# Performance work log

Measured on AMD Instinct MI355X. Metric: run time of the kernel, lower is better.

## Reference

```python
import jax, jax.numpy as jnp
import numpy as np

B, S, D, M = 4, 4096, 2048, 512

def _xavier(k, shape):
    return jax.random.normal(k, shape, jnp.float32) * np.float32(np.sqrt(2.0 / (shape[0] + shape[1])))

def setup_inputs() -> dict:
    key = jax.random.key(0)
    ks = jax.random.split(key, 6)
    return dict(
        x=jax.random.normal(ks[0], (B, S, D), jnp.float32),
        memory_state=jnp.zeros((B, M), jnp.float32),
        Wk=_xavier(ks[1], (M, D)), bk=jnp.zeros((M,), jnp.float32),
        Wv=_xavier(ks[2], (M, D)), bv=jnp.zeros((M,), jnp.float32),
        Wg=_xavier(ks[3], (D, D + M)), bg=jnp.zeros((D,), jnp.float32),
        time_decay=jax.random.normal(ks[4], (M,), jnp.float32) * 0.01,
        time_first=jax.random.normal(ks[5], (M,), jnp.float32) * 0.01,
    )

def reference(x, memory_state, Wk, bk, Wv, bv, Wg, bg, time_decay, time_first):
    # decay in (0.1, 1.0) per channel
    td = jax.nn.sigmoid(time_decay) * 0.9 + 0.1          # (M,)
    tf = jax.nn.sigmoid(time_first)                      # (M,)
    # k is computed but never used in the source forward; kept for FLOP parity
    k = jnp.einsum('bsd,md->bsm', x, Wk) + bk
    v = jnp.einsum('bsd,md->bsm', x, Wv) + bv            # (B,S,M)
    # sum_{j<=i} td^(i-j) * v_j  ==  linear recurrence s_i = td*s_{i-1} + v_i
    def step(s, v_t):
        s = td * s + v_t
        return s, s
    _, wv = jax.lax.scan(step, jnp.zeros((x.shape[0], td.shape[0]), x.dtype),
                         jnp.swapaxes(v, 0, 1))          # (S,B,M)
    wv = jnp.swapaxes(wv, 0, 1) + memory_state[:, None, :] * tf  # (B,S,M)
    next_memory_state = wv[:, -1]                        # taken before dropout (eval: identity)
    combined = jnp.concatenate([x, wv], axis=-1)         # (B,S,D+M)
    out = x + jnp.einsum('bse,de->bsd', combined, Wg) + bg
    return out, next_memory_state
```

## Files before the change

kernel.cpp:

```cpp
#include <hip/hip_runtime.h>
#include <hip/hip_bf16.h>
#include <stdint.h>

#define B_ 4
#define S_ 4096
#define D_ 2048
#define M_ 512
#define E_ (D_ + M_)
#define BS_ (B_ * S_)
#define CH_ 32
#define CL_ 128

typedef __attribute__((ext_vector_type(8))) short short8;
typedef __attribute__((ext_vector_type(4))) short short4e;
typedef __attribute__((ext_vector_type(4))) float float4e;

__device__ __forceinline__ unsigned short f2bf(float f) {
    unsigned int u = __float_as_uint(f);
    u = (u + 0x7fffu + ((u >> 16) & 1u)) >> 16;
    return (unsigned short)u;
}

__device__ __forceinline__ float sigmoidf(float x) {
    return 1.0f / (1.0f + expf(-x));
}

__device__ __forceinline__ void load_lds16(const unsigned short* g, unsigned short* l) {
    __builtin_amdgcn_global_load_lds(
        (const __attribute__((address_space(1))) unsigned int*)g,
        (__attribute__((address_space(3))) unsigned int*)l,
        16, 0, 0);
}

__global__ void conv_x_kernel(const float* __restrict__ x, unsigned short* __restrict__ comb) {
    int i = blockIdx.x * blockDim.x + threadIdx.x;
    const int n4 = BS_ * D_ / 4;
    const int stride = gridDim.x * blockDim.x;
    for (; i < n4; i += stride) {
        int flat = i << 2;
        int row = flat >> 11;
        int col = flat & (D_ - 1);
        float4 xv = ((const float4*)x)[i];
        short4e o = { (short)f2bf(xv.x), (short)f2bf(xv.y),
                      (short)f2bf(xv.z), (short)f2bf(xv.w) };
        *(short4e*)(comb + (size_t)row * E_ + col) = o;
    }
}

__global__ void conv_gen(const float* __restrict__ in, unsigned short* __restrict__ out, int n4) {
    int i = blockIdx.x * blockDim.x + threadIdx.x;
    const int stride = gridDim.x * blockDim.x;
    for (; i < n4; i += stride) {
        float4 xv = ((const float4*)in)[i];
        short4e o = { (short)f2bf(xv.x), (short)f2bf(xv.y),
                      (short)f2bf(xv.z), (short)f2bf(xv.w) };
        ((short4e*)out)[i] = o;
    }
}

template<bool ADDX>
__global__ __launch_bounds__(256) void gemm_bt(
    const unsigned short* __restrict__ A, int lda,
    const unsigned short* __restrict__ Bm, int ldb,
    float* __restrict__ C, int ldc,
    const float* __restrict__ bias,
    const float* __restrict__ xres,
    int K)
{
    __shared__ unsigned short As[128 * 64];
    __shared__ unsigned short Bs[128 * 64];

    const int tid  = threadIdx.x;
    const int lane = tid & 63;
    const int wave = __builtin_amdgcn_readfirstlane(tid >> 6);
    const int bm0  = blockIdx.x * 128;
    const int bn0  = blockIdx.y * 128;
    const int wm   = wave & 1;
    const int wn   = wave >> 1;
    const int lm   = lane & 15;
    const int quad = lane >> 4;

    const unsigned short* ag[4];
    const unsigned short* bgp[4];
    unsigned short* al[4];
    unsigned short* bl[4];
#pragma unroll
    for (int i = 0; i < 4; ++i) {
        int g = i * 256 + tid;
        int r = g >> 3, c = g & 7;
        int cg = c ^ (r & 7);
        ag[i]  = A  + (size_t)(bm0 + r) * lda + cg * 8;
        bgp[i] = Bm + (size_t)(bn0 + r) * ldb + cg * 8;
        int lg = i * 256 + wave * 64;
        al[i] = As + lg * 8;
        bl[i] = Bs + lg * 8;
    }

    float4e acc[4][4];
    const float4e zero = {0.f, 0.f, 0.f, 0.f};
#pragma unroll
    for (int i = 0; i < 4; ++i)
#pragma unroll
        for (int j = 0; j < 4; ++j) acc[i][j] = zero;

    for (int k0 = 0; k0 < K; k0 += 64) {
#pragma unroll
        for (int i = 0; i < 4; ++i) {
            load_lds16(ag[i]  + k0, al[i]);
            load_lds16(bgp[i] + k0, bl[i]);
        }
        __syncthreads();
#pragma unroll
        for (int kk = 0; kk < 2; ++kk) {
            short8 af[4], bf[4];
#pragma unroll
            for (int i = 0; i < 4; ++i) {
                int ra = wm * 64 + i * 16 + lm;
                af[i] = *(const short8*)(As + ra * 64 + (((kk * 4 + quad) ^ (ra & 7)) * 8));
                int rb = wn * 64 + i * 16 + lm;
                bf[i] = *(const short8*)(Bs + rb * 64 + (((kk * 4 + quad) ^ (rb & 7)) * 8));
            }
#pragma unroll
            for (int i = 0; i < 4; ++i)
#pragma unroll
                for (int j = 0; j < 4; ++j)
                    acc[i][j] = __builtin_amdgcn_mfma_f32_16x16x32_bf16(af[i], bf[j], acc[i][j], 0, 0, 0);
        }
        __syncthreads();
    }

#pragma unroll
    for (int i = 0; i < 4; ++i) {
#pragma unroll
        for (int j = 0; j < 4; ++j) {
            int row = bm0 + wm * 64 + i * 16 + quad * 4;
            int col = bn0 + wn * 64 + j * 16 + lm;
            float bb = bias[col];
#pragma unroll
            for (int r = 0; r < 4; ++r) {
                size_t idx = (size_t)(row + r) * ldc + col;
                float val = acc[i][j][r] + bb;
                if (ADDX) val += xres[idx];
                C[idx] = val;
            }
        }
    }
}

__global__ void scan_p1(const float* __restrict__ v, const float* __restrict__ tdp,
                        float* __restrict__ Ebuf) {
    int tid = blockIdx.x * blockDim.x + threadIdx.x;
    int m = tid & (M_ - 1);
    int c = (tid >> 9) & (CH_ - 1);
    int b = tid >> 14;
    float td = 0.9f * sigmoidf(tdp[m]) + 0.1f;
    const float* vp = v + (size_t)(b * S_ + c * CL_) * M_ + m;
    float s = 0.f;
#pragma unroll 4
    for (int t = 0; t < CL_; ++t) s = td * s + vp[(size_t)t * M_];
    Ebuf[(b * CH_ + c) * M_ + m] = s;
}

__global__ void scan_p2(const float* __restrict__ tdp, const float* __restrict__ Ebuf,
                        float* __restrict__ Sbuf) {
    int tid = blockIdx.x * blockDim.x + threadIdx.x;
    int m = tid & (M_ - 1);
    int b = tid >> 9;
    float td = 0.9f * sigmoidf(tdp[m]) + 0.1f;
    float a = td;
#pragma unroll
    for (int i = 0; i < 7; ++i) a *= a;
    float s = 0.f;
    for (int c = 0; c < CH_; ++c) {
        Sbuf[(b * CH_ + c) * M_ + m] = s;
        s = a * s + Ebuf[(b * CH_ + c) * M_ + m];
    }
}

__global__ void scan_p3(const float* __restrict__ v, const float* __restrict__ tdp,
                        const float* __restrict__ tfp, const float* __restrict__ ms,
                        const float* __restrict__ Sbuf, unsigned short* __restrict__ comb,
                        float* __restrict__ out_state) {
    int tid = blockIdx.x * blockDim.x + threadIdx.x;
    int m = tid & (M_ - 1);
    int c = (tid >> 9) & (CH_ - 1);
    int b = tid >> 14;
    float td  = 0.9f * sigmoidf(tdp[m]) + 0.1f;
    float add = ms[b * M_ + m] * sigmoidf(tfp[m]);
    float s   = Sbuf[(b * CH_ + c) * M_ + m];
    const float* vp = v + (size_t)(b * S_ + c * CL_) * M_ + m;
    unsigned short* cp = comb + (size_t)(b * S_ + c * CL_) * E_ + D_ + m;
    float w = 0.f;
#pragma unroll 4
    for (int t = 0; t < CL_; ++t) {
        s = td * s + vp[(size_t)t * M_];
        w = s + add;
        cp[(size_t)t * E_] = f2bf(w);
    }
    if (c == CH_ - 1) out_state[b * M_ + m] = w;
}

extern "C" void kernel_launch(void* const* d_in, const int* in_sizes, int n_in,
                              void* d_out, int out_size, void* d_ws, size_t ws_size,
                              hipStream_t stream) {
    const float* x    = (const float*)d_in[0];
    const float* ms   = (const float*)d_in[1];
    const float* Wv   = (const float*)d_in[4];
    const float* bv   = (const float*)d_in[5];
    const float* Wg   = (const float*)d_in[6];
    const float* bg   = (const float*)d_in[7];
    const float* tdec = (const float*)d_in[8];
    const float* tfir = (const float*)d_in[9];

    float* out       = (float*)d_out;
    float* out_state = out + (size_t)BS_ * D_;

    char* ws = (char*)d_ws;
    size_t off = 0;
    unsigned short* comb = (unsigned short*)(ws + off); off += (size_t)BS_ * E_ * 2;
    float*          vbuf = (float*)(ws + off);          off += (size_t)BS_ * M_ * 4;
    unsigned short* Wvb  = (unsigned short*)(ws + off); off += (size_t)M_ * D_ * 2;
    unsigned short* Wgb  = (unsigned short*)(ws + off); off += (size_t)D_ * E_ * 2;
    float*          Ebuf = (float*)(ws + off);          off += (size_t)B_ * CH_ * M_ * 4;
    float*          Sbuf = (float*)(ws + off);          off += (size_t)B_ * CH_ * M_ * 4;

    conv_x_kernel<<<4096, 256, 0, stream>>>(x, comb);
    conv_gen<<<512, 256, 0, stream>>>(Wv, Wvb, M_ * D_ / 4);
    conv_gen<<<2048, 256, 0, stream>>>(Wg, Wgb, D_ * E_ / 4);

    gemm_bt<false><<<dim3(BS_ / 128, M_ / 128), 256, 0, stream>>>(
        comb, E_, Wvb, D_, vbuf, M_, bv, nullptr, D_);

    scan_p1<<<(B_ * CH_ * M_) / 256, 256, 0, stream>>>(vbuf, tdec, Ebuf);
    scan_p2<<<(B_ * M_) / 256, 256, 0, stream>>>(tdec, Ebuf, Sbuf);
    scan_p3<<<(B_ * CH_ * M_) / 256, 256, 0, stream>>>(vbuf, tdec, tfir, ms, Sbuf, comb, out_state);

    gemm_bt<true><<<dim3(BS_ / 128, D_ / 128), 256, 0, stream>>>(
        comb, E_, Wgb, E_, out, D_, bg, x, E_);
}
```

Before: 581.5 us.

## Store v in bf16, merge weight casts, fold scan pass 2, read residual from bf16

Several changes ship together. The v projection now writes bf16 instead of fp32 and uses 128x64 tiles, which halves the traffic the scan kernels read. The two weight-cast kernels become one launch, and the scan's middle pass is removed by having each chunk recompute its carry-in prefix. The output GEMM reads the x residual from the bf16 copy in comb instead of fp32 x, and its grid is reordered so N varies fastest. These cut memory traffic and launches, but rounding v and the residual x to bf16 lowers accuracy; the residual loss in particular may break tolerance.

```diff
diff --git a/kernel.cpp b/kernel.cpp
--- a/kernel.cpp
+++ b/kernel.cpp
@@ -20,7 +20,9 @@
     u = (u + 0x7fffu + ((u >> 16) & 1u)) >> 16;
     return (unsigned short)u;
 }
-
+__device__ __forceinline__ float bf2f(unsigned short h) {
+    return __uint_as_float(((unsigned int)h) << 16);
+}
 __device__ __forceinline__ float sigmoidf(float x) {
     return 1.0f / (1.0f + expf(-x));
 }
@@ -47,155 +49,165 @@
     }
 }
 
-__global__ void conv_gen(const float* __restrict__ in, unsigned short* __restrict__ out, int n4) {
+__global__ void conv_w_kernel(const float* __restrict__ Wv, unsigned short* __restrict__ Wvb,
+                              const float* __restrict__ Wg, unsigned short* __restrict__ Wgb) {
+    const int nv4 = M_ * D_ / 4;
+    const int ng4 = D_ * E_ / 4;
     int i = blockIdx.x * blockDim.x + threadIdx.x;
     const int stride = gridDim.x * blockDim.x;
-    for (; i < n4; i += stride) {
-        float4 xv = ((const float4*)in)[i];
+    for (; i < nv4 + ng4; i += stride) {
+        const float* in;
+        unsigned short* out;
+        int j;
+        if (i < nv4) { in = Wv; out = Wvb; j = i; }
+        else         { in = Wg; out = Wgb; j = i - nv4; }
+        float4 xv = ((const float4*)in)[j];
         short4e o = { (short)f2bf(xv.x), (short)f2bf(xv.y),
                       (short)f2bf(xv.z), (short)f2bf(xv.w) };
-        ((short4e*)out)[i] = o;
-    }
-}
-
-template<bool ADDX>
+        ((short4e*)out)[j] = o;
+    }
+}
+
+template<int BM, int BN, bool ADDX, bool OUT_BF16>
 __global__ __launch_bounds__(256) void gemm_bt(
     const unsigned short* __restrict__ A, int lda,
     const unsigned short* __restrict__ Bm, int ldb,
-    float* __restrict__ C, int ldc,
+    void* __restrict__ Cv, int ldc,
     const float* __restrict__ bias,
-    const float* __restrict__ xres,
+    const unsigned short* __restrict__ resid, int resid_ld,
     int K)
 {
-    __shared__ unsigned short As[128 * 64];
-    __shared__ unsigned short Bs[128 * 64];
+    constexpr int MI = BM / 32;
+    constexpr int NJ = BN / 32;
+    constexpr int NGA = BM / 32;
+    constexpr int NGB = BN / 32;
+
+    __shared__ unsigned short As[BM * 64];
+    __shared__ unsigned short Bs[BN * 64];
 
     const int tid  = threadIdx.x;
     const int lane = tid & 63;
     const int wave = __builtin_amdgcn_readfirstlane(tid >> 6);
-    const int bm0  = blockIdx.x * 128;
-    const int bn0  = blockIdx.y * 128;
+    const int bn0  = blockIdx.x * BN;
+    const int bm0  = blockIdx.y * BM;
     const int wm   = wave & 1;
     const int wn   = wave >> 1;
     const int lm   = lane & 15;
     const int quad = lane >> 4;
 
-    const unsigned short* ag[4];
-    const unsigned short* bgp[4];
-    unsigned short* al[4];
-    unsigned short* bl[4];
-#pragma unroll
-    for (int i = 0; i < 4; ++i) {
+    const unsigned short* ag[NGA];
+    unsigned short* al[NGA];
+#pragma unroll
+    for (int i = 0; i < NGA; ++i) {
         int g = i * 256 + tid;
         int r = g >> 3, c = g & 7;
         int cg = c ^ (r & 7);
-        ag[i]  = A  + (size_t)(bm0 + r) * lda + cg * 8;
+        ag[i] = A + (size_t)(bm0 + r) * lda + cg * 8;
+        al[i] = As + (i * 256 + wave * 64) * 8;
+    }
+    const unsigned short* bgp[NGB];
+    unsigned short* bl[NGB];
+#pragma unroll
+    for (int i = 0; i < NGB; ++i) {
+        int g = i * 256 + tid;
+        int r = g >> 3, c = g & 7;
+        int cg = c ^ (r & 7);
         bgp[i] = Bm + (size_t)(bn0 + r) * ldb + cg * 8;
-        int lg = i * 256 + wave * 64;
-        al[i] = As + lg * 8;
-        bl[i] = Bs + lg * 8;
-    }
-
-    float4e acc[4][4];
+        bl[i] = Bs + (i * 256 + wave * 64) * 8;
+    }
+
+    float4e acc[MI][NJ];
     const float4e zero = {0.f, 0.f, 0.f, 0.f};
 #pragma unroll
-    for (int i = 0; i < 4; ++i)
-#pragma unroll
-        for (int j = 0; j < 4; ++j) acc[i][j] = zero;
+    for (int i = 0; i < MI; ++i)
+#pragma unroll
+        for (int j = 0; j < NJ; ++j) acc[i][j] = zero;
 
     for (int k0 = 0; k0 < K; k0 += 64) {
 #pragma unroll
-        for (int i = 0; i < 4; ++i) {
-            load_lds16(ag[i]  + k0, al[i]);
-            load_lds16(bgp[i] + k0, bl[i]);
-        }
+        for (int i = 0; i < NGA; ++i) load_lds16(ag[i] + k0, al[i]);
+#pragma unroll
+        for (int i = 0; i < NGB; ++i) load_lds16(bgp[i] + k0, bl[i]);
         __syncthreads();
 #pragma unroll
         for (int kk = 0; kk < 2; ++kk) {
-            short8 af[4], bf[4];
-#pragma unroll
-            for (int i = 0; i < 4; ++i) {
-                int ra = wm * 64 + i * 16 + lm;
+            short8 af[MI], bf[NJ];
+#pragma unroll
+            for (int i = 0; i < MI; ++i) {
+                int ra = wm * (BM / 2) + i * 16 + lm;
                 af[i] = *(const short8*)(As + ra * 64 + (((kk * 4 + quad) ^ (ra & 7)) * 8));
-                int rb = wn * 64 + i * 16 + lm;
-                bf[i] = *(const short8*)(Bs + rb * 64 + (((kk * 4 + quad) ^ (rb & 7)) * 8));
             }
 #pragma unroll
-            for (int i = 0; i < 4; ++i)
-#pragma unroll
-                for (int j = 0; j < 4; ++j)
+            for (int j = 0; j < NJ; ++j) {
+                int rb = wn * (BN / 2) + j * 16 + lm;
+                bf[j] = *(const short8*)(Bs + rb * 64 + (((kk * 4 + quad) ^ (rb & 7)) * 8));
+            }
+#pragma unroll
+            for (int i = 0; i < MI; ++i)
+#pragma unroll
+                for (int j = 0; j < NJ; ++j)
                     acc[i][j] = __builtin_amdgcn_mfma_f32_16x16x32_bf16(af[i], bf[j], acc[i][j], 0, 0, 0);
         }
         __syncthreads();
     }
 
 #pragma unroll
-    for (int i = 0; i < 4; ++i) {
-#pragma unroll
-        for (int j = 0; j < 4; ++j) {
-            int row = bm0 + wm * 64 + i * 16 + quad * 4;
-            int col = bn0 + wn * 64 + j * 16 + lm;
+    for (int i = 0; i < MI; ++i) {
+#pragma unroll
+        for (int j = 0; j < NJ; ++j) {
+            int row = bm0 + wm * (BM / 2) + i * 16 + quad * 4;
+            int col = bn0 + wn * (BN / 2) + j * 16 + lm;
             float bb = bias[col];
 #pragma unroll
             for (int r = 0; r < 4; ++r) {
                 size_t idx = (size_t)(row + r) * ldc + col;
                 float val = acc[i][j][r] + bb;
-                if (ADDX) val += xres[idx];
-                C[idx] = val;
+                if (ADDX) val += bf2f(resid[(size_t)(row + r) * resid_ld + col]);
+                if (OUT_BF16) ((unsigned short*)Cv)[idx] = f2bf(val);
+                else          ((float*)Cv)[idx] = val;
             }
         }
     }
 }
 
-__global__ void scan_p1(const float* __restrict__ v, const float* __restrict__ tdp,
+__global__ void scan_p1(const unsigned short* __restrict__ v, const float* __restrict__ tdp,
                         float* __restrict__ Ebuf) {
     int tid = blockIdx.x * blockDim.x + threadIdx.x;
     int m = tid & (M_ - 1);
     int c = (tid >> 9) & (CH_ - 1);
     int b = tid >> 14;
     float td = 0.9f * sigmoidf(tdp[m]) + 0.1f;
-    const float* vp = v + (size_t)(b * S_ + c * CL_) * M_ + m;
+    const unsigned short* vp = v + (size_t)(b * S_ + c * CL_) * M_ + m;
     float s = 0.f;
 #pragma unroll 4
-    for (int t = 0; t < CL_; ++t) s = td * s + vp[(size_t)t * M_];
+    for (int t = 0; t < CL_; ++t) s = td * s + bf2f(vp[(size_t)t * M_]);
     Ebuf[(b * CH_ + c) * M_ + m] = s;
 }
 
-__global__ void scan_p2(const float* __restrict__ tdp, const float* __restrict__ Ebuf,
-                        float* __restrict__ Sbuf) {
-    int tid = blockIdx.x * blockDim.x + threadIdx.x;
-    int m = tid & (M_ - 1);
-    int b = tid >> 9;
-    float td = 0.9f * sigmoidf(tdp[m]) + 0.1f;
-    float a = td;
-#pragma unroll
-    for (int i = 0; i < 7; ++i) a *= a;
-    float s = 0.f;
-    for (int c = 0; c < CH_; ++c) {
-        Sbuf[(b * CH_ + c) * M_ + m] = s;
-        s = a * s + Ebuf[(b * CH_ + c) * M_ + m];
-    }
-}
-
-__global__ void scan_p3(const float* __restrict__ v, const float* __restrict__ tdp,
+__global__ void scan_p3(const unsigned short* __restrict__ v, const float* __restrict__ tdp,
                         const float* __restrict__ tfp, const float* __restrict__ ms,
-                        const float* __restrict__ Sbuf, unsigned short* __restrict__ comb,
+                        const float* __restrict__ Ebuf, unsigned short* __restrict__ comb,
                         float* __restrict__ out_state) {
     int tid = blockIdx.x * blockDim.x + threadIdx.x;
     int m = tid & (M_ - 1);
     int c = (tid >> 9) & (CH_ - 1);
     int b = tid >> 14;
     float td  = 0.9f * sigmoidf(tdp[m]) + 0.1f;
+    float a = td;
+#pragma unroll
+    for (int i = 0; i < 7; ++i) a *= a;
+    float s = 0.f;
+    for (int cp = 0; cp < c; ++cp)
+        s = a * s + Ebuf[(b * CH_ + cp) * M_ + m];
     float add = ms[b * M_ + m] * sigmoidf(tfp[m]);
-    float s   = Sbuf[(b * CH_ + c) * M_ + m];
-    const float* vp = v + (size_t)(b * S_ + c * CL_) * M_ + m;
-    unsigned short* cp = comb + (size_t)(b * S_ + c * CL_) * E_ + D_ + m;
+    const unsigned short* vp = v + (size_t)(b * S_ + c * CL_) * M_ + m;
+    unsigned short* cp_ = comb + (size_t)(b * S_ + c * CL_) * E_ + D_ + m;
     float w = 0.f;
 #pragma unroll 4
     for (int t = 0; t < CL_; ++t) {
-        s = td * s + vp[(size_t)t * M_];
+        s = td * s + bf2f(vp[(size_t)t * M_]);
         w = s + add;
-        cp[(size_t)t * E_] = f2bf(w);
+        cp_[(size_t)t * E_] = f2bf(w);
     }
     if (c == CH_ - 1) out_state[b * M_ + m] = w;
 }
@@ -218,23 +230,20 @@
     char* ws = (char*)d_ws;
     size_t off = 0;
     unsigned short* comb = (unsigned short*)(ws + off); off += (size_t)BS_ * E_ * 2;
-    float*          vbuf = (float*)(ws + off);          off += (size_t)BS_ * M_ * 4;
+    unsigned short* vbuf = (unsigned short*)(ws + off); off += (size_t)BS_ * M_ * 2;
     unsigned short* Wvb  = (unsigned short*)(ws + off); off += (size_t)M_ * D_ * 2;
     unsigned short* Wgb  = (unsigned short*)(ws + off); off += (size_t)D_ * E_ * 2;
     float*          Ebuf = (float*)(ws + off);          off += (size_t)B_ * CH_ * M_ * 4;
-    float*          Sbuf = (float*)(ws + off);          off += (size_t)B_ * CH_ * M_ * 4;
 
     conv_x_kernel<<<4096, 256, 0, stream>>>(x, comb);
-    conv_gen<<<512, 256, 0, stream>>>(Wv, Wvb, M_ * D_ / 4);
-    conv_gen<<<2048, 256, 0, stream>>>(Wg, Wgb, D_ * E_ / 4);
-
-    gemm_bt<false><<<dim3(BS_ / 128, M_ / 128), 256, 0, stream>>>(
-        comb, E_, Wvb, D_, vbuf, M_, bv, nullptr, D_);
+    conv_w_kernel<<<1536, 256, 0, stream>>>(Wv, Wvb, Wg, Wgb);
+
+    gemm_bt<128, 64, false, true><<<dim3(M_ / 64, BS_ / 128), 256, 0, stream>>>(
+        comb, E_, Wvb, D_, vbuf, M_, bv, nullptr, 0, D_);
 
     scan_p1<<<(B_ * CH_ * M_) / 256, 256, 0, stream>>>(vbuf, tdec, Ebuf);
-    scan_p2<<<(B_ * M_) / 256, 256, 0, stream>>>(tdec, Ebuf, Sbuf);
-    scan_p3<<<(B_ * CH_ * M_) / 256, 256, 0, stream>>>(vbuf, tdec, tfir, ms, Sbuf, comb, out_state);
-
-    gemm_bt<true><<<dim3(BS_ / 128, D_ / 128), 256, 0, stream>>>(
-        comb, E_, Wgb, E_, out, D_, bg, x, E_);
-}
+    scan_p3<<<(B_ * CH_ * M_) / 256, 256, 0, stream>>>(vbuf, tdec, tfir, ms, Ebuf, comb, out_state);
+
+    gemm_bt<128, 128, true, false><<<dim3(D_ / 128, BS_ / 128), 256, 0, stream>>>(
+        comb, E_, Wgb, E_, out, D_, bg, comb, E_, E_);
+}
```

New measurement: 573.2 us. About the same (-1.4%).
